# Optimization experiments

Hardware: AMD Instinct MI355X
Metric: run time of the kernel (lower is better)

Reference implementation:

```python
import jax, jax.numpy as jnp
import numpy as np

B, X, Y, Z, CIN = 4, 64, 64, 64, 32
COUT = 32
MX, MY, MZ = 16, 16, 16


def setup_inputs() -> dict:
    key = jax.random.key(0)
    k1, k2, k3 = jax.random.split(key, 3)
    x = jax.random.normal(k1, (B, X, Y, Z, CIN), dtype=jnp.float32)
    # Glorot-uniform-like scale for (in, out, mx, my, mz) weights
    fan = CIN + COUT
    lim = np.sqrt(6.0 / fan).astype(np.float32)
    w_real = jax.random.uniform(k2, (CIN, COUT, MX, MY, MZ), minval=-lim, maxval=lim, dtype=jnp.float32)
    w_imag = jax.random.uniform(k3, (CIN, COUT, MX, MY, MZ), minval=-lim, maxval=lim, dtype=jnp.float32)
    return {"x": x, "w_real": w_real, "w_imag": w_imag}


def reference(x, w_real, w_imag):
    # tf.signal.fft3d transforms the innermost 3 axes of the 5D input:
    # x is [B, X, Y, Z, C] so the FFT runs over (Y, Z, C) -- faithful to source.
    x_ft = jnp.fft.fftn(x.astype(jnp.complex64), axes=(-3, -2, -1))
    x_ft = jnp.transpose(x_ft, (0, 4, 1, 2, 3))            # [B, C, X, Y, Z]
    mx, my, mz = w_real.shape[2], w_real.shape[3], w_real.shape[4]
    x_crop = x_ft[:, :, :mx, :my, :mz]                     # [B, Cin, mx, my, mz]
    w = jax.lax.complex(w_real, w_imag)                    # [Cin, Cout, mx, my, mz]
    out_ft = jnp.einsum('bixyz,ioxyz->boxyz', x_crop, w)   # [B, Cout, mx, my, mz]
    sx, sy, sz = x.shape[1], x.shape[2], x.shape[3]
    out_ft = jnp.pad(out_ft, ((0, 0), (0, 0), (0, sx - mx), (0, sy - my), (0, sz - mz)))
    out_ft = jnp.transpose(out_ft, (0, 2, 3, 4, 1))        # [B, X, Y, Z, Cout]
    x_out = jnp.fft.ifftn(out_ft, axes=(-3, -2, -1))
    return jnp.real(x_out)
```

## Files before the change

kernel.cpp:

```cpp
#include <hip/hip_runtime.h>
#include <math.h>

#define PI_F 3.14159265358979323846f


__global__ __launch_bounds__(256) void k_dft_z(const float* __restrict__ x,
                                               float2* __restrict__ T1) {
    int bid = blockIdx.x;
    int y  = bid & 63;
    int xx = (bid >> 6) & 15;
    int b  = bid >> 10;
    __shared__ float  sx[2048];
    __shared__ float2 tw[1024];
    const float* src = x + (size_t)((b * 64 + xx) * 64 + y) * 2048;
    for (int t = threadIdx.x; t < 2048; t += 256) sx[t] = src[t];
    const float c = -2.0f * PI_F / 64.0f;
    for (int t = threadIdx.x; t < 1024; t += 256) {
        int kz = t >> 6, z = t & 63;
        float s, cc; sincosf(c * (float)((kz * z) & 63), &s, &cc);
        tw[t] = make_float2(cc, s);
    }
    __syncthreads();
    float2* dst = T1 + (size_t)((b * 16 + xx) * 64 + y) * 512;
    for (int o = threadIdx.x; o < 512; o += 256) {
        int kz = o >> 5, i = o & 31;
        float ar = 0.f, ai = 0.f;
        for (int z = 0; z < 64; ++z) {
            float  v = sx[z * 32 + i];
            float2 t = tw[kz * 64 + z];
            ar = fmaf(v, t.x, ar);
            ai = fmaf(v, t.y, ai);
        }
        dst[o] = make_float2(ar, ai);
    }
}

__global__ __launch_bounds__(256) void k_dft_y(const float2* __restrict__ T1,
                                               float2* __restrict__ XH) {
    int bid = blockIdx.x;
    int kz = bid & 15;
    int bx = bid >> 4;
    __shared__ float2 sT[2048];
    __shared__ float2 tw[1024];
    const float2* src = T1 + (size_t)bx * 64 * 512 + kz * 32;
    for (int t = threadIdx.x; t < 2048; t += 256) {
        int y = t >> 5, i = t & 31;
        sT[t] = src[(size_t)y * 512 + i];
    }
    const float c = -2.0f * PI_F / 64.0f;
    for (int t = threadIdx.x; t < 1024; t += 256) {
        int ky = t >> 6, y = t & 63;
        float s, cc; sincosf(c * (float)((ky * y) & 63), &s, &cc);
        tw[t] = make_float2(cc, s);
    }
    __syncthreads();
    float2* dst = XH + (size_t)bx * 8192 + kz * 32;
    for (int o = threadIdx.x; o < 512; o += 256) {
        int ky = o >> 5, i = o & 31;
        float ar = 0.f, ai = 0.f;
        for (int y = 0; y < 64; ++y) {
            float2 a = sT[y * 32 + i];
            float2 t = tw[ky * 64 + y];
            ar = fmaf(a.x, t.x, fmaf(-a.y, t.y, ar));
            ai = fmaf(a.x, t.y, fmaf( a.y, t.x, ai));
        }
        dst[(size_t)ky * 512 + i] = make_float2(ar, ai);
    }
}

__global__ __launch_bounds__(256) void k_dft_i(const float2* __restrict__ XH,
                                               float2* __restrict__ X2) {
    int bid = blockIdx.x;
    int ky = bid & 15;
    int xx = (bid >> 4) & 15;
    int b  = bid >> 8;
    __shared__ float2 sX[16 * 33];
    __shared__ float2 tw[32 * 33];
    const float2* src = XH + (size_t)bid * 512;
    for (int t = threadIdx.x; t < 512; t += 256) {
        int kz = t >> 5, i = t & 31;
        sX[kz * 33 + i] = src[t];
    }
    const float c = -2.0f * PI_F / 32.0f;
    for (int t = threadIdx.x; t < 1024; t += 256) {
        int ki = t >> 5, i = t & 31;
        float s, cc; sincosf(c * (float)((ki * i) & 31), &s, &cc);
        tw[ki * 33 + i] = make_float2(cc, s);
    }
    __syncthreads();
    for (int o = threadIdx.x; o < 512; o += 256) {
        int ki = o >> 4, kz = o & 15;
        float ar = 0.f, ai = 0.f;
        for (int i = 0; i < 32; ++i) {
            float2 a = sX[kz * 33 + i];
            float2 t = tw[ki * 33 + i];
            ar = fmaf(a.x, t.x, fmaf(-a.y, t.y, ar));
            ai = fmaf(a.x, t.y, fmaf( a.y, t.x, ai));
        }
        X2[((size_t)(b * 32 + ki) * 16 + xx) * 256 + ky * 16 + kz] = make_float2(ar, ai);
    }
}

__global__ __launch_bounds__(256) void k_wmul(const float2* __restrict__ X2,
                                              const float* __restrict__ wr,
                                              const float* __restrict__ wi,
                                              float2* __restrict__ F) {
    int bid = blockIdx.x;
    int ky = bid & 15, xx = bid >> 4;
    __shared__ float2 sX[4 * 32 * 16];
    for (int t = threadIdx.x; t < 2048; t += 256) {
        int b = t >> 9, ki = (t >> 4) & 31, kz = t & 15;
        sX[t] = X2[((size_t)(b * 32 + ki) * 16 + xx) * 256 + ky * 16 + kz];
    }
    __syncthreads();
    int kz = threadIdx.x & 15;
    int o0 = threadIdx.x >> 4;
    float2 acc[2][4];
    for (int h = 0; h < 2; ++h)
        for (int b = 0; b < 4; ++b) acc[h][b] = make_float2(0.f, 0.f);
    int wbase = xx * 256 + ky * 16 + kz;
    for (int ki = 0; ki < 32; ++ki) {
        for (int h = 0; h < 2; ++h) {
            int o = o0 + 16 * h;
            float wrv = wr[(size_t)(ki * 32 + o) * 4096 + wbase];
            float wiv = wi[(size_t)(ki * 32 + o) * 4096 + wbase];
            for (int b = 0; b < 4; ++b) {
                float2 a = sX[(b * 32 + ki) * 16 + kz];
                acc[h][b].x = fmaf(a.x, wrv, fmaf(-a.y, wiv, acc[h][b].x));
                acc[h][b].y = fmaf(a.x, wiv, fmaf( a.y, wrv, acc[h][b].y));
            }
        }
    }
    for (int h = 0; h < 2; ++h) {
        int o = o0 + 16 * h;
        for (int b = 0; b < 4; ++b)
            F[((size_t)((b * 16 + xx) * 16 + ky) * 16 + kz) * 32 + o] = acc[h][b];
    }
}

__global__ __launch_bounds__(256) void k_idft_o(const float2* __restrict__ F,
                                                float2* __restrict__ G) {
    int bid = blockIdx.x;
    __shared__ float2 sF[16 * 33];
    __shared__ float2 tw[32 * 33];
    const float2* src = F + (size_t)bid * 512;
    for (int t = threadIdx.x; t < 512; t += 256) {
        int kz = t >> 5, o = t & 31;
        sF[kz * 33 + o] = src[t];
    }
    const float c = 2.0f * PI_F / 32.0f;
    for (int t = threadIdx.x; t < 1024; t += 256) {
        int co = t >> 5, o = t & 31;
        float s, cc; sincosf(c * (float)((co * o) & 31), &s, &cc);
        tw[co * 33 + o] = make_float2(cc, s);
    }
    __syncthreads();
    float2* dst = G + (size_t)bid * 512;
    for (int t = threadIdx.x; t < 512; t += 256) {
        int kz = t >> 5, co = t & 31;
        float ar = 0.f, ai = 0.f;
        for (int o = 0; o < 32; ++o) {
            float2 a  = sF[kz * 33 + o];
            float2 tt = tw[co * 33 + o];
            ar = fmaf(a.x, tt.x, fmaf(-a.y, tt.y, ar));
            ai = fmaf(a.x, tt.y, fmaf( a.y, tt.x, ai));
        }
        dst[kz * 32 + co] = make_float2(ar, ai);
    }
}

__global__ __launch_bounds__(256) void k_idft_z(const float2* __restrict__ G,
                                                float2* __restrict__ H) {
    int bid = blockIdx.x;
    __shared__ float2 sG[512];
    __shared__ float2 tw[1024];
    const float2* src = G + (size_t)bid * 512;
    for (int t = threadIdx.x; t < 512; t += 256) sG[t] = src[t];
    const float c = 2.0f * PI_F / 64.0f;
    for (int t = threadIdx.x; t < 1024; t += 256) {
        int z = t >> 4, kz = t & 15;
        float s, cc; sincosf(c * (float)((kz * z) & 63), &s, &cc);
        tw[t] = make_float2(cc, s);
    }
    __syncthreads();
    float2* dst = H + (size_t)bid * 2048;
    int co = threadIdx.x & 31;
    int zg = threadIdx.x >> 5;
    for (int j = 0; j < 8; ++j) {
        int z = zg * 8 + j;
        float ar = 0.f, ai = 0.f;
        for (int kz = 0; kz < 16; ++kz) {
            float2 a  = sG[kz * 32 + co];
            float2 tt = tw[z * 16 + kz];
            ar = fmaf(a.x, tt.x, fmaf(-a.y, tt.y, ar));
            ai = fmaf(a.x, tt.y, fmaf( a.y, tt.x, ai));
        }
        dst[z * 32 + co] = make_float2(ar, ai);
    }
}

__global__ __launch_bounds__(256) void k_idft_y(const float2* __restrict__ H,
                                                float* __restrict__ out) {
    int bid = blockIdx.x;
    int zc = bid & 7;
    int xx = (bid >> 3) & 63;
    int b  = bid >> 9;
    float* dst = out + (size_t)(b * 64 + xx) * 131072 + zc * 256;
    if (xx >= 16) {
        for (int q = threadIdx.x; q < 4096; q += 256) {
            int y = q >> 6, r = q & 63;
            ((float4*)(dst + (size_t)y * 2048))[r] = make_float4(0.f, 0.f, 0.f, 0.f);
        }
        return;
    }
    __shared__ float2 sH[4096];
    __shared__ float2 twy[1024];
    const float2* src = H + (size_t)(b * 16 + xx) * 32768 + zc * 256;
    for (int t = threadIdx.x; t < 4096; t += 256) {
        int ky = t >> 8, r = t & 255;
        sH[t] = src[(size_t)ky * 2048 + r];
    }
    const float c = 2.0f * PI_F / 64.0f;
    for (int t = threadIdx.x; t < 1024; t += 256) {
        int y = t >> 4, ky = t & 15;
        float s, cc; sincosf(c * (float)((ky * y) & 63), &s, &cc);
        twy[t] = make_float2(cc, s);
    }
    __syncthreads();
    const float scale = 1.0f / 131072.0f;
    int r = threadIdx.x;
    for (int y = 0; y < 64; ++y) {
        float ar = 0.f;
        for (int ky = 0; ky < 16; ++ky) {
            float2 a  = sH[ky * 256 + r];
            float2 tt = twy[y * 16 + ky];
            ar = fmaf(a.x, tt.x, fmaf(-a.y, tt.y, ar));
        }
        dst[(size_t)y * 2048 + r] = ar * scale;
    }
}

extern "C" void kernel_launch(void* const* d_in, const int* in_sizes, int n_in,
                              void* d_out, int out_size, void* d_ws, size_t ws_size,
                              hipStream_t stream) {
    const float* x  = (const float*)d_in[0];
    const float* wr = (const float*)d_in[1];
    const float* wi = (const float*)d_in[2];
    float* out = (float*)d_out;
    char*  ws  = (char*)d_ws;
    float2* A = (float2*)ws;
    float2* Bv = (float2*)(ws + (size_t)2097152 * 8);
    float2* Cv = (float2*)(ws + (size_t)2097152 * 8 + (size_t)524288 * 8);

    k_dft_z <<<4096, 256, 0, stream>>>(x, A);
    k_dft_y <<<1024, 256, 0, stream>>>(A, Bv);
    k_dft_i <<<1024, 256, 0, stream>>>(Bv, Cv);
    k_wmul  <<< 256, 256, 0, stream>>>(Cv, wr, wi, Bv);
    k_idft_o<<<1024, 256, 0, stream>>>(Bv, Cv);
    k_idft_z<<<1024, 256, 0, stream>>>(Cv, A);
    k_idft_y<<<2048, 256, 0, stream>>>(A, out);
}
```

Measured before the change: 337.2 us.

## Fuse DFT stages into four kernels with register-tiled outer-product loops

```diff
diff --git a/kernel.cpp b/kernel.cpp
--- a/kernel.cpp
+++ b/kernel.cpp
@@ -7,236 +7,303 @@
 __global__ __launch_bounds__(256) void k_dft_z(const float* __restrict__ x,
                                                float2* __restrict__ T1) {
     int bid = blockIdx.x;
-    int y  = bid & 63;
-    int xx = (bid >> 6) & 15;
-    int b  = bid >> 10;
-    __shared__ float  sx[2048];
-    __shared__ float2 tw[1024];
-    const float* src = x + (size_t)((b * 64 + xx) * 64 + y) * 2048;
-    for (int t = threadIdx.x; t < 2048; t += 256) sx[t] = src[t];
-    const float c = -2.0f * PI_F / 64.0f;
+    int yg = bid & 7, xx = (bid >> 3) & 15, b = bid >> 7;
+    __shared__ float  sx[16384];
+    __shared__ float2 twt[1024];
+    float4* sx4 = (float4*)sx;
+    const float4* src4 = (const float4*)(x + (size_t)((b * 64 + xx) * 64 + yg * 8) * 2048);
+    #pragma unroll
+    for (int t = threadIdx.x; t < 4096; t += 256) sx4[t] = src4[t];
+    const float cn = -2.0f * PI_F / 64.0f;
     for (int t = threadIdx.x; t < 1024; t += 256) {
-        int kz = t >> 6, z = t & 63;
-        float s, cc; sincosf(c * (float)((kz * z) & 63), &s, &cc);
-        tw[t] = make_float2(cc, s);
-    }
-    __syncthreads();
+        int z = t >> 4, kz = t & 15;
+        float s, c; sincosf(cn * (float)((z * kz) & 63), &s, &c);
+        twt[t] = make_float2(c, s);
+    }
+    __syncthreads();
+    int ig = threadIdx.x & 3, kz2 = (threadIdx.x >> 2) & 7, y8 = threadIdx.x >> 5;
+    float ar0[8], ai0[8], ar1[8], ai1[8];
+    #pragma unroll
+    for (int j = 0; j < 8; j++) { ar0[j] = ai0[j] = ar1[j] = ai1[j] = 0.f; }
+    const float4* twv = (const float4*)twt;
+    #pragma unroll 4
+    for (int z = 0; z < 64; z++) {
+        float4 va = sx4[(y8 * 64 + z) * 8 + ig * 2];
+        float4 vb = sx4[(y8 * 64 + z) * 8 + ig * 2 + 1];
+        float4 tp = twv[z * 8 + kz2];
+        float v[8] = {va.x, va.y, va.z, va.w, vb.x, vb.y, vb.z, vb.w};
+        #pragma unroll
+        for (int j = 0; j < 8; j++) {
+            ar0[j] = fmaf(v[j], tp.x, ar0[j]);
+            ai0[j] = fmaf(v[j], tp.y, ai0[j]);
+            ar1[j] = fmaf(v[j], tp.z, ar1[j]);
+            ai1[j] = fmaf(v[j], tp.w, ai1[j]);
+        }
+    }
+    int y = yg * 8 + y8, kz0 = kz2 * 2, i0 = ig * 8;
     float2* dst = T1 + (size_t)((b * 16 + xx) * 64 + y) * 512;
-    for (int o = threadIdx.x; o < 512; o += 256) {
-        int kz = o >> 5, i = o & 31;
-        float ar = 0.f, ai = 0.f;
-        for (int z = 0; z < 64; ++z) {
-            float  v = sx[z * 32 + i];
-            float2 t = tw[kz * 64 + z];
-            ar = fmaf(v, t.x, ar);
-            ai = fmaf(v, t.y, ai);
-        }
-        dst[o] = make_float2(ar, ai);
-    }
+    float4* d0 = (float4*)(dst + kz0 * 32 + i0);
+    d0[0] = make_float4(ar0[0], ai0[0], ar0[1], ai0[1]);
+    d0[1] = make_float4(ar0[2], ai0[2], ar0[3], ai0[3]);
+    d0[2] = make_float4(ar0[4], ai0[4], ar0[5], ai0[5]);
+    d0[3] = make_float4(ar0[6], ai0[6], ar0[7], ai0[7]);
+    float4* d1 = (float4*)(dst + (kz0 + 1) * 32 + i0);
+    d1[0] = make_float4(ar1[0], ai1[0], ar1[1], ai1[1]);
+    d1[1] = make_float4(ar1[2], ai1[2], ar1[3], ai1[3]);
+    d1[2] = make_float4(ar1[4], ai1[4], ar1[5], ai1[5]);
+    d1[3] = make_float4(ar1[6], ai1[6], ar1[7], ai1[7]);
 }
 
 __global__ __launch_bounds__(256) void k_dft_y(const float2* __restrict__ T1,
                                                float2* __restrict__ XH) {
     int bid = blockIdx.x;
-    int kz = bid & 15;
-    int bx = bid >> 4;
-    __shared__ float2 sT[2048];
-    __shared__ float2 tw[1024];
-    const float2* src = T1 + (size_t)bx * 64 * 512 + kz * 32;
+    int kzg = bid & 3, xx = (bid >> 2) & 15, b = bid >> 6;
+    __shared__ float2 sT[4 * 2178];
+    __shared__ float2 twt[1024];
+    float4* sT4 = (float4*)sT;
+    const float4* Tg4 = (const float4*)T1;
+    size_t gbase = (size_t)(b * 16 + xx) * 64 * 256 + (size_t)kzg * 64;
+    for (int t = threadIdx.x; t < 4096; t += 256) {
+        int y = t >> 6, kz4 = (t >> 4) & 3, i4 = t & 15;
+        sT4[kz4 * 1089 + y * 17 + i4] = Tg4[gbase + (size_t)y * 256 + kz4 * 16 + i4];
+    }
+    const float cn = -2.0f * PI_F / 64.0f;
+    for (int t = threadIdx.x; t < 1024; t += 256) {
+        int y = t >> 4, ky = t & 15;
+        float s, c; sincosf(cn * (float)((y * ky) & 63), &s, &c);
+        twt[t] = make_float2(c, s);
+    }
+    __syncthreads();
+    int ig = threadIdx.x & 7, ky2 = (threadIdx.x >> 3) & 7, kz4 = threadIdx.x >> 6;
+    float ar[2][4], ai[2][4];
+    #pragma unroll
+    for (int h = 0; h < 2; h++)
+        #pragma unroll
+        for (int j = 0; j < 4; j++) { ar[h][j] = ai[h][j] = 0.f; }
+    const float4* twv = (const float4*)twt;
+    #pragma unroll 4
+    for (int y = 0; y < 64; y++) {
+        float4 a01 = sT4[kz4 * 1089 + y * 17 + ig * 2];
+        float4 a23 = sT4[kz4 * 1089 + y * 17 + ig * 2 + 1];
+        float4 tp = twv[y * 8 + ky2];
+        float xr[4] = {a01.x, a01.z, a23.x, a23.z};
+        float xi[4] = {a01.y, a01.w, a23.y, a23.w};
+        #pragma unroll
+        for (int j = 0; j < 4; j++) {
+            ar[0][j] += xr[j] * tp.x - xi[j] * tp.y;
+            ai[0][j] += xr[j] * tp.y + xi[j] * tp.x;
+            ar[1][j] += xr[j] * tp.z - xi[j] * tp.w;
+            ai[1][j] += xr[j] * tp.w + xi[j] * tp.z;
+        }
+    }
+    int kz = kzg * 4 + kz4, i0 = ig * 4;
+    #pragma unroll
+    for (int h = 0; h < 2; h++) {
+        int ky = ky2 * 2 + h;
+        float2* dp = XH + (((size_t)(b * 16 + xx) * 16 + ky) * 16 + kz) * 32 + i0;
+        ((float4*)dp)[0] = make_float4(ar[h][0], ai[h][0], ar[h][1], ai[h][1]);
+        ((float4*)dp)[1] = make_float4(ar[h][2], ai[h][2], ar[h][3], ai[h][3]);
+    }
+}
+
+__global__ __launch_bounds__(256) void k_mid(const float2* __restrict__ XH,
+                                             const float* __restrict__ wr,
+                                             const float* __restrict__ wi,
+                                             float2* __restrict__ G) {
+    int bid = blockIdx.x;
+    int ky = bid & 15, xx = bid >> 4;
+    __shared__ float2 sA[4 * 528];
+    __shared__ float2 sB[4 * 576];
+    __shared__ float2 twt[1024];
     for (int t = threadIdx.x; t < 2048; t += 256) {
-        int y = t >> 5, i = t & 31;
-        sT[t] = src[(size_t)y * 512 + i];
-    }
-    const float c = -2.0f * PI_F / 64.0f;
+        int b = t >> 9, kz = (t >> 5) & 15, i = t & 31;
+        sA[b * 528 + kz * 33 + i] =
+            XH[(((size_t)(b * 16 + xx) * 16 + ky) * 16 + kz) * 32 + i];
+    }
+    const float cn32 = -2.0f * PI_F / 32.0f;
+    for (int t = threadIdx.x; t < 1024; t += 256) {
+        int m = t >> 5, k = t & 31;
+        float s, c; sincosf(cn32 * (float)((m * k) & 31), &s, &c);
+        twt[t] = make_float2(c, s);
+    }
+    __syncthreads();
+    const float4* twv = (const float4*)twt;
+    {
+        int kz = threadIdx.x & 15, ki8 = (threadIdx.x >> 4) & 3, b = threadIdx.x >> 6;
+        float xr[8], xi[8];
+        #pragma unroll
+        for (int j = 0; j < 8; j++) { xr[j] = xi[j] = 0.f; }
+        #pragma unroll 4
+        for (int i = 0; i < 32; i++) {
+            float2 a = sA[b * 528 + kz * 33 + i];
+            #pragma unroll
+            for (int k = 0; k < 4; k++) {
+                float4 tp = twv[i * 16 + ki8 * 4 + k];
+                xr[2 * k]     += a.x * tp.x - a.y * tp.y;
+                xi[2 * k]     += a.x * tp.y + a.y * tp.x;
+                xr[2 * k + 1] += a.x * tp.z - a.y * tp.w;
+                xi[2 * k + 1] += a.x * tp.w + a.y * tp.z;
+            }
+        }
+        #pragma unroll
+        for (int j = 0; j < 8; j++)
+            sB[b * 576 + (ki8 * 8 + j) * 18 + kz] = make_float2(xr[j], xi[j]);
+    }
+    __syncthreads();
+    {
+        int kzg = threadIdx.x & 3, o2 = (threadIdx.x >> 2) & 15, b = threadIdx.x >> 6;
+        int wbase = xx * 256 + ky * 16 + kzg * 4;
+        float Fr[2][4], Fi[2][4];
+        #pragma unroll
+        for (int h = 0; h < 2; h++)
+            #pragma unroll
+            for (int q = 0; q < 4; q++) { Fr[h][q] = Fi[h][q] = 0.f; }
+        const float4* sB4 = (const float4*)sB;
+        #pragma unroll 4
+        for (int ki = 0; ki < 32; ki++) {
+            float4 a01 = sB4[b * 288 + ki * 9 + kzg * 2];
+            float4 a23 = sB4[b * 288 + ki * 9 + kzg * 2 + 1];
+            float xr[4] = {a01.x, a01.z, a23.x, a23.z};
+            float xi[4] = {a01.y, a01.w, a23.y, a23.w};
+            #pragma unroll
+            for (int ol = 0; ol < 2; ol++) {
+                int o = o2 * 2 + ol;
+                float4 w4r = *(const float4*)(wr + (size_t)(ki * 32 + o) * 4096 + wbase);
+                float4 w4i = *(const float4*)(wi + (size_t)(ki * 32 + o) * 4096 + wbase);
+                float wrv[4] = {w4r.x, w4r.y, w4r.z, w4r.w};
+                float wiv[4] = {w4i.x, w4i.y, w4i.z, w4i.w};
+                #pragma unroll
+                for (int q = 0; q < 4; q++) {
+                    Fr[ol][q] += xr[q] * wrv[q] - xi[q] * wiv[q];
+                    Fi[ol][q] += xr[q] * wiv[q] + xi[q] * wrv[q];
+                }
+            }
+        }
+        #pragma unroll
+        for (int ol = 0; ol < 2; ol++) {
+            int o = o2 * 2 + ol;
+            #pragma unroll
+            for (int q = 0; q < 4; q++) {
+                int kz = kzg * 4 + q;
+                sA[b * 528 + kz * 33 + o] = make_float2(Fr[ol][q], Fi[ol][q]);
+            }
+        }
+    }
+    __syncthreads();
+    {
+        int kz = threadIdx.x & 15, co8 = (threadIdx.x >> 4) & 3, b = threadIdx.x >> 6;
+        float gr[8], gi[8];
+        #pragma unroll
+        for (int j = 0; j < 8; j++) { gr[j] = gi[j] = 0.f; }
+        #pragma unroll 4
+        for (int o = 0; o < 32; o++) {
+            float2 f = sA[b * 528 + kz * 33 + o];
+            #pragma unroll
+            for (int k = 0; k < 4; k++) {
+                float4 tp = twv[o * 16 + co8 * 4 + k];
+                gr[2 * k]     += f.x * tp.x + f.y * tp.y;
+                gi[2 * k]     += f.y * tp.x - f.x * tp.y;
+                gr[2 * k + 1] += f.x * tp.z + f.y * tp.w;
+                gi[2 * k + 1] += f.y * tp.z - f.x * tp.w;
+            }
+        }
+        float2* dp = G + (((size_t)(b * 16 + xx) * 16 + ky) * 16 + kz) * 32 + co8 * 8;
+        ((float4*)dp)[0] = make_float4(gr[0], gi[0], gr[1], gi[1]);
+        ((float4*)dp)[1] = make_float4(gr[2], gi[2], gr[3], gi[3]);
+        ((float4*)dp)[2] = make_float4(gr[4], gi[4], gr[5], gi[5]);
+        ((float4*)dp)[3] = make_float4(gr[6], gi[6], gr[7], gi[7]);
+    }
+}
+
+__global__ __launch_bounds__(256) void k_idft_zy(const float2* __restrict__ G,
+                                                 float* __restrict__ out) {
+    int bid = blockIdx.x;
+    int zc = bid & 7, xx = (bid >> 3) & 63, b = bid >> 9;
+    float* dstb = out + (size_t)(b * 64 + xx) * 131072;
+    if (xx >= 16) {
+        float4* d4 = (float4*)dstb;
+        for (int t = threadIdx.x; t < 4096; t += 256) {
+            int y = t >> 6, r = t & 63;
+            d4[(size_t)y * 512 + zc * 64 + r] = make_float4(0.f, 0.f, 0.f, 0.f);
+        }
+        return;
+    }
+    __shared__ float2 sH[128 * 34];
+    __shared__ float2 twy[1024];
+    __shared__ float2 twz[8 * 17];
+    const float cp = 2.0f * PI_F / 64.0f;
     for (int t = threadIdx.x; t < 1024; t += 256) {
         int ky = t >> 6, y = t & 63;
-        float s, cc; sincosf(c * (float)((ky * y) & 63), &s, &cc);
-        tw[t] = make_float2(cc, s);
-    }
-    __syncthreads();
-    float2* dst = XH + (size_t)bx * 8192 + kz * 32;
-    for (int o = threadIdx.x; o < 512; o += 256) {
-        int ky = o >> 5, i = o & 31;
-        float ar = 0.f, ai = 0.f;
-        for (int y = 0; y < 64; ++y) {
-            float2 a = sT[y * 32 + i];
-            float2 t = tw[ky * 64 + y];
-            ar = fmaf(a.x, t.x, fmaf(-a.y, t.y, ar));
-            ai = fmaf(a.x, t.y, fmaf( a.y, t.x, ai));
-        }
-        dst[(size_t)ky * 512 + i] = make_float2(ar, ai);
-    }
-}
-
-__global__ __launch_bounds__(256) void k_dft_i(const float2* __restrict__ XH,
-                                               float2* __restrict__ X2) {
-    int bid = blockIdx.x;
-    int ky = bid & 15;
-    int xx = (bid >> 4) & 15;
-    int b  = bid >> 8;
-    __shared__ float2 sX[16 * 33];
-    __shared__ float2 tw[32 * 33];
-    const float2* src = XH + (size_t)bid * 512;
-    for (int t = threadIdx.x; t < 512; t += 256) {
-        int kz = t >> 5, i = t & 31;
-        sX[kz * 33 + i] = src[t];
-    }
-    const float c = -2.0f * PI_F / 32.0f;
-    for (int t = threadIdx.x; t < 1024; t += 256) {
-        int ki = t >> 5, i = t & 31;
-        float s, cc; sincosf(c * (float)((ki * i) & 31), &s, &cc);
-        tw[ki * 33 + i] = make_float2(cc, s);
-    }
-    __syncthreads();
-    for (int o = threadIdx.x; o < 512; o += 256) {
-        int ki = o >> 4, kz = o & 15;
-        float ar = 0.f, ai = 0.f;
-        for (int i = 0; i < 32; ++i) {
-            float2 a = sX[kz * 33 + i];
-            float2 t = tw[ki * 33 + i];
-            ar = fmaf(a.x, t.x, fmaf(-a.y, t.y, ar));
-            ai = fmaf(a.x, t.y, fmaf( a.y, t.x, ai));
-        }
-        X2[((size_t)(b * 32 + ki) * 16 + xx) * 256 + ky * 16 + kz] = make_float2(ar, ai);
-    }
-}
-
-__global__ __launch_bounds__(256) void k_wmul(const float2* __restrict__ X2,
-                                              const float* __restrict__ wr,
-                                              const float* __restrict__ wi,
-                                              float2* __restrict__ F) {
-    int bid = blockIdx.x;
-    int ky = bid & 15, xx = bid >> 4;
-    __shared__ float2 sX[4 * 32 * 16];
-    for (int t = threadIdx.x; t < 2048; t += 256) {
-        int b = t >> 9, ki = (t >> 4) & 31, kz = t & 15;
-        sX[t] = X2[((size_t)(b * 32 + ki) * 16 + xx) * 256 + ky * 16 + kz];
-    }
-    __syncthreads();
-    int kz = threadIdx.x & 15;
-    int o0 = threadIdx.x >> 4;
-    float2 acc[2][4];
-    for (int h = 0; h < 2; ++h)
-        for (int b = 0; b < 4; ++b) acc[h][b] = make_float2(0.f, 0.f);
-    int wbase = xx * 256 + ky * 16 + kz;
-    for (int ki = 0; ki < 32; ++ki) {
-        for (int h = 0; h < 2; ++h) {
-            int o = o0 + 16 * h;
-            float wrv = wr[(size_t)(ki * 32 + o) * 4096 + wbase];
-            float wiv = wi[(size_t)(ki * 32 + o) * 4096 + wbase];
-            for (int b = 0; b < 4; ++b) {
-                float2 a = sX[(b * 32 + ki) * 16 + kz];
-                acc[h][b].x = fmaf(a.x, wrv, fmaf(-a.y, wiv, acc[h][b].x));
-                acc[h][b].y = fmaf(a.x, wiv, fmaf( a.y, wrv, acc[h][b].y));
-            }
-        }
-    }
-    for (int h = 0; h < 2; ++h) {
-        int o = o0 + 16 * h;
-        for (int b = 0; b < 4; ++b)
-            F[((size_t)((b * 16 + xx) * 16 + ky) * 16 + kz) * 32 + o] = acc[h][b];
-    }
-}
-
-__global__ __launch_bounds__(256) void k_idft_o(const float2* __restrict__ F,
-                                                float2* __restrict__ G) {
-    int bid = blockIdx.x;
-    __shared__ float2 sF[16 * 33];
-    __shared__ float2 tw[32 * 33];
-    const float2* src = F + (size_t)bid * 512;
-    for (int t = threadIdx.x; t < 512; t += 256) {
-        int kz = t >> 5, o = t & 31;
-        sF[kz * 33 + o] = src[t];
-    }
-    const float c = 2.0f * PI_F / 32.0f;
-    for (int t = threadIdx.x; t < 1024; t += 256) {
-        int co = t >> 5, o = t & 31;
-        float s, cc; sincosf(c * (float)((co * o) & 31), &s, &cc);
-        tw[co * 33 + o] = make_float2(cc, s);
-    }
-    __syncthreads();
-    float2* dst = G + (size_t)bid * 512;
-    for (int t = threadIdx.x; t < 512; t += 256) {
-        int kz = t >> 5, co = t & 31;
-        float ar = 0.f, ai = 0.f;
-        for (int o = 0; o < 32; ++o) {
-            float2 a  = sF[kz * 33 + o];
-            float2 tt = tw[co * 33 + o];
-            ar = fmaf(a.x, tt.x, fmaf(-a.y, tt.y, ar));
-            ai = fmaf(a.x, tt.y, fmaf( a.y, tt.x, ai));
-        }
-        dst[kz * 32 + co] = make_float2(ar, ai);
-    }
-}
-
-__global__ __launch_bounds__(256) void k_idft_z(const float2* __restrict__ G,
-                                                float2* __restrict__ H) {
-    int bid = blockIdx.x;
-    __shared__ float2 sG[512];
-    __shared__ float2 tw[1024];
-    const float2* src = G + (size_t)bid * 512;
-    for (int t = threadIdx.x; t < 512; t += 256) sG[t] = src[t];
-    const float c = 2.0f * PI_F / 64.0f;
-    for (int t = threadIdx.x; t < 1024; t += 256) {
-        int z = t >> 4, kz = t & 15;
-        float s, cc; sincosf(c * (float)((kz * z) & 63), &s, &cc);
-        tw[t] = make_float2(cc, s);
-    }
-    __syncthreads();
-    float2* dst = H + (size_t)bid * 2048;
-    int co = threadIdx.x & 31;
-    int zg = threadIdx.x >> 5;
-    for (int j = 0; j < 8; ++j) {
-        int z = zg * 8 + j;
-        float ar = 0.f, ai = 0.f;
-        for (int kz = 0; kz < 16; ++kz) {
-            float2 a  = sG[kz * 32 + co];
-            float2 tt = tw[z * 16 + kz];
-            ar = fmaf(a.x, tt.x, fmaf(-a.y, tt.y, ar));
-            ai = fmaf(a.x, tt.y, fmaf( a.y, tt.x, ai));
-        }
-        dst[z * 32 + co] = make_float2(ar, ai);
-    }
-}
-
-__global__ __launch_bounds__(256) void k_idft_y(const float2* __restrict__ H,
-                                                float* __restrict__ out) {
-    int bid = blockIdx.x;
-    int zc = bid & 7;
-    int xx = (bid >> 3) & 63;
-    int b  = bid >> 9;
-    float* dst = out + (size_t)(b * 64 + xx) * 131072 + zc * 256;
-    if (xx >= 16) {
-        for (int q = threadIdx.x; q < 4096; q += 256) {
-            int y = q >> 6, r = q & 63;
-            ((float4*)(dst + (size_t)y * 2048))[r] = make_float4(0.f, 0.f, 0.f, 0.f);
-        }
-        return;
-    }
-    __shared__ float2 sH[4096];
-    __shared__ float2 twy[1024];
-    const float2* src = H + (size_t)(b * 16 + xx) * 32768 + zc * 256;
-    for (int t = threadIdx.x; t < 4096; t += 256) {
-        int ky = t >> 8, r = t & 255;
-        sH[t] = src[(size_t)ky * 2048 + r];
-    }
-    const float c = 2.0f * PI_F / 64.0f;
-    for (int t = threadIdx.x; t < 1024; t += 256) {
-        int y = t >> 4, ky = t & 15;
-        float s, cc; sincosf(c * (float)((ky * y) & 63), &s, &cc);
-        twy[t] = make_float2(cc, s);
-    }
-    __syncthreads();
-    const float scale = 1.0f / 131072.0f;
-    int r = threadIdx.x;
-    for (int y = 0; y < 64; ++y) {
-        float ar = 0.f;
-        for (int ky = 0; ky < 16; ++ky) {
-            float2 a  = sH[ky * 256 + r];
-            float2 tt = twy[y * 16 + ky];
-            ar = fmaf(a.x, tt.x, fmaf(-a.y, tt.y, ar));
-        }
-        dst[(size_t)y * 2048 + r] = ar * scale;
+        float s, c; sincosf(cp * (float)((ky * y) & 63), &s, &c);
+        twy[t] = make_float2(c, s);
+    }
+    if (threadIdx.x < 128) {
+        int dz = threadIdx.x >> 4, kz = threadIdx.x & 15;
+        int z = zc * 8 + dz;
+        float s, c; sincosf(cp * (float)((kz * z) & 63), &s, &c);
+        twz[dz * 17 + kz] = make_float2(c, s);
+    }
+    __syncthreads();
+    {
+        int coh = threadIdx.x & 1, dz = (threadIdx.x >> 1) & 7, ky = threadIdx.x >> 4;
+        const float2* Gb = G + ((size_t)(b * 16 + xx) * 16 + ky) * 512 + coh * 16;
+        float Hr[16], Hi[16];
+        #pragma unroll
+        for (int j = 0; j < 16; j++) { Hr[j] = Hi[j] = 0.f; }
+        #pragma unroll 2
+        for (int kz = 0; kz < 16; kz++) {
+            float2 tz = twz[dz * 17 + kz];
+            #pragma unroll
+            for (int k = 0; k < 8; k++) {
+                float4 g = *(const float4*)(Gb + kz * 32 + k * 2);
+                Hr[2 * k]     += g.x * tz.x - g.y * tz.y;
+                Hi[2 * k]     += g.x * tz.y + g.y * tz.x;
+                Hr[2 * k + 1] += g.z * tz.x - g.w * tz.y;
+                Hi[2 * k + 1] += g.z * tz.y + g.w * tz.x;
+            }
+        }
+        float2* hp = sH + (ky * 8 + dz) * 34 + coh * 16;
+        #pragma unroll
+        for (int k = 0; k < 8; k++)
+            *(float4*)(hp + k * 2) = make_float4(Hr[2 * k], Hi[2 * k], Hr[2 * k + 1], Hi[2 * k + 1]);
+    }
+    __syncthreads();
+    {
+        int cog = threadIdx.x & 3, dz = (threadIdx.x >> 2) & 7, yg = threadIdx.x >> 5;
+        float acc[8][8];
+        #pragma unroll
+        for (int yl = 0; yl < 8; yl++)
+            #pragma unroll
+            for (int cl = 0; cl < 8; cl++) acc[yl][cl] = 0.f;
+        const float4* twy4 = (const float4*)twy;
+        const float4* sH4 = (const float4*)sH;
+        for (int ky = 0; ky < 16; ky++) {
+            float4 t0 = twy4[ky * 32 + yg * 4 + 0];
+            float4 t1 = twy4[ky * 32 + yg * 4 + 1];
+            float4 t2 = twy4[ky * 32 + yg * 4 + 2];
+            float4 t3 = twy4[ky * 32 + yg * 4 + 3];
+            float4 h0 = sH4[(ky * 8 + dz) * 17 + cog * 4 + 0];
+            float4 h1 = sH4[(ky * 8 + dz) * 17 + cog * 4 + 1];
+            float4 h2 = sH4[(ky * 8 + dz) * 17 + cog * 4 + 2];
+            float4 h3 = sH4[(ky * 8 + dz) * 17 + cog * 4 + 3];
+            float tc[8] = {t0.x, t0.z, t1.x, t1.z, t2.x, t2.z, t3.x, t3.z};
+            float ts[8] = {t0.y, t0.w, t1.y, t1.w, t2.y, t2.w, t3.y, t3.w};
+            float hr[8] = {h0.x, h0.z, h1.x, h1.z, h2.x, h2.z, h3.x, h3.z};
+            float hi[8] = {h0.y, h0.w, h1.y, h1.w, h2.y, h2.w, h3.y, h3.w};
+            #pragma unroll
+            for (int yl = 0; yl < 8; yl++)
+                #pragma unroll
+                for (int cl = 0; cl < 8; cl++)
+                    acc[yl][cl] += tc[yl] * hr[cl] - ts[yl] * hi[cl];
+        }
+        const float sc = 1.0f / 131072.0f;
+        #pragma unroll
+        for (int yl = 0; yl < 8; yl++) {
+            int y = yg * 8 + yl;
+            float4* d4 = (float4*)(dstb + ((size_t)y * 64 + zc * 8 + dz) * 32 + cog * 8);
+            d4[0] = make_float4(acc[yl][0] * sc, acc[yl][1] * sc, acc[yl][2] * sc, acc[yl][3] * sc);
+            d4[1] = make_float4(acc[yl][4] * sc, acc[yl][5] * sc, acc[yl][6] * sc, acc[yl][7] * sc);
+        }
     }
 }
 
@@ -248,15 +315,12 @@
     const float* wi = (const float*)d_in[2];
     float* out = (float*)d_out;
     char*  ws  = (char*)d_ws;
-    float2* A = (float2*)ws;
-    float2* Bv = (float2*)(ws + (size_t)2097152 * 8);
-    float2* Cv = (float2*)(ws + (size_t)2097152 * 8 + (size_t)524288 * 8);
-
-    k_dft_z <<<4096, 256, 0, stream>>>(x, A);
-    k_dft_y <<<1024, 256, 0, stream>>>(A, Bv);
-    k_dft_i <<<1024, 256, 0, stream>>>(Bv, Cv);
-    k_wmul  <<< 256, 256, 0, stream>>>(Cv, wr, wi, Bv);
-    k_idft_o<<<1024, 256, 0, stream>>>(Bv, Cv);
-    k_idft_z<<<1024, 256, 0, stream>>>(Cv, A);
-    k_idft_y<<<2048, 256, 0, stream>>>(A, out);
-}
+    float2* T1 = (float2*)ws;
+    float2* XH = (float2*)(ws + (size_t)16777216);
+    float2* Gb = (float2*)(ws + (size_t)16777216 + 4194304);
+
+    k_dft_z  <<< 512, 256, 0, stream>>>(x, T1);
+    k_dft_y  <<< 256, 256, 0, stream>>>(T1, XH);
+    k_mid    <<< 256, 256, 0, stream>>>(XH, wr, wi, Gb);
+    k_idft_zy<<<2048, 256, 0, stream>>>(Gb, out);
+}
```

New measurement: 293.0 us. 1.15x faster.
